# Performance work log

Measured on AMD Instinct MI355X. Metric: run time of the kernel, lower is better.

The kernel has to match this reference:

```python
import jax, jax.numpy as jnp
import numpy as np
from jax import lax

B, S, H = 2, 1024, 1024
I = 512            # moe_intermediate_size
E = 32             # n_routed_experts
TOP_K = 4
N_GROUP = 4
TOPK_GROUP = 2
SCALE = 2.5        # routed_scaling_factor
N_SHARED = 2
SH_I = I * N_SHARED


def setup_inputs() -> dict:
    key = jax.random.key(0)
    ks = jax.random.split(key, 10)
    std = 0.02
    return {
        "hidden_states": jax.random.normal(ks[0], (B, S, H), jnp.float32),
        "router_weight": jax.random.normal(ks[1], (E, H), jnp.float32) * std,
        "router_bias": jnp.zeros((E,), jnp.float32),
        "gate_w": jax.random.normal(ks[2], (E, I, H), jnp.float32) * std,
        "up_w": jax.random.normal(ks[3], (E, I, H), jnp.float32) * std,
        "down_w": jax.random.normal(ks[4], (E, H, I), jnp.float32) * std,
        "shared_gate_w": jax.random.normal(ks[5], (SH_I, H), jnp.float32) * std,
        "shared_up_w": jax.random.normal(ks[6], (SH_I, H), jnp.float32) * std,
        "shared_down_w": jax.random.normal(ks[7], (H, SH_I), jnp.float32) * std,
    }


def _route(tokens, router_weight, router_bias):
    # tokens: [T, H] -> topk_idx [T, K] int, topk_weight [T, K] f32
    logits = tokens.astype(jnp.float32) @ router_weight.astype(jnp.float32).T  # [T, E]
    scores = jax.nn.sigmoid(logits)
    sfc = scores + router_bias[None, :]
    T = tokens.shape[0]
    # group scores: sum of top-2 per group
    grp = sfc.reshape(T, N_GROUP, E // N_GROUP)
    group_scores = lax.top_k(grp, 2)[0].sum(-1)                 # [T, n_group]
    _, gidx = lax.top_k(group_scores, TOPK_GROUP)               # [T, topk_group]
    gmask = jax.nn.one_hot(gidx, N_GROUP, dtype=sfc.dtype).sum(1)  # [T, n_group]
    smask = jnp.broadcast_to(gmask[:, :, None], (T, N_GROUP, E // N_GROUP)).reshape(T, E)
    tmp = jnp.where(smask > 0, sfc, 0.0)
    _, topk_idx = lax.top_k(tmp, TOP_K)                         # [T, K]
    topk_w = jnp.take_along_axis(scores, topk_idx, axis=1)
    topk_w = topk_w / (topk_w.sum(-1, keepdims=True) + 1e-20)   # norm_topk_prob
    topk_w = topk_w * SCALE
    return topk_idx, topk_w


def reference(hidden_states, router_weight, router_bias, gate_w, up_w, down_w,
              shared_gate_w, shared_up_w, shared_down_w):
    tokens = hidden_states.reshape(-1, H)                       # [T, H]
    topk_idx, topk_w = _route(tokens, router_weight, router_bias)
    # dense all-expert SwiGLU
    gate_vals = jax.nn.silu(jnp.einsum('th,eih->tei', tokens, gate_w))
    up_vals = jnp.einsum('th,eih->tei', tokens, up_w)
    hidden_vals = gate_vals * up_vals                           # [T, E, I]
    expert_out = jnp.einsum('tei,ehi->teh', hidden_vals, down_w)  # [T, E, H]
    sel = jnp.take_along_axis(expert_out, topk_idx[:, :, None], axis=1)  # [T, K, H]
    mixed = (sel * topk_w[:, :, None].astype(sel.dtype)).sum(1)
    mixed = mixed.reshape(hidden_states.shape)
    # shared experts (dense SwiGLU MLP)
    sg = jax.nn.silu(jnp.einsum('bsh,ih->bsi', hidden_states, shared_gate_w))
    su = jnp.einsum('bsh,ih->bsi', hidden_states, shared_up_w)
    shared = jnp.einsum('bsi,hi->bsh', sg * su, shared_down_w)
    return mixed + shared
```

## Files before the change

### kernel.cpp

```cpp
#include <hip/hip_runtime.h>
#include <hip/hip_bf16.h>
#include <math.h>

#define HD 1024
#define ID 512
#define NE 32
#define NT 2048
#define NG 4
#define SHI 1024
#define SCALE 2.5f

#define BN 64
#define BK 32
#define LDA 40

typedef __bf16 bf16_t;
typedef __attribute__((ext_vector_type(8))) __bf16 bf16x8;
typedef __attribute__((ext_vector_type(4))) __bf16 bf16x4;
typedef __attribute__((ext_vector_type(4))) float f32x4;

__device__ __forceinline__ void gld16(const bf16_t* g, bf16_t* l) {
    __builtin_amdgcn_global_load_lds(
        (__attribute__((address_space(1))) void*)g,
        (__attribute__((address_space(3))) void*)l,
        16, 0, 0);
}

#define CH_G 2097152LL
#define CH_S 131072LL
#define CH_H 262144LL
#define CH_TOT (3*CH_G + 3*CH_S + CH_H)

__global__ void __launch_bounds__(256) convert_all(
    const float* __restrict__ g, const float* __restrict__ u, const float* __restrict__ d,
    const float* __restrict__ sg, const float* __restrict__ su, const float* __restrict__ sd,
    const float* __restrict__ hs, bf16_t* __restrict__ dst)
{
    for (long long c = blockIdx.x * 256LL + threadIdx.x; c < CH_TOT; c += (long long)gridDim.x * 256LL) {
        const float* src;
        long long r = c;
        if (r < CH_G)                   src = g  + (size_t)r * 8;
        else if ((r -= CH_G) < CH_G)    src = u  + (size_t)r * 8;
        else if ((r -= CH_G) < CH_G)    src = d  + (size_t)r * 8;
        else if ((r -= CH_G) < CH_S)    src = sg + (size_t)r * 8;
        else if ((r -= CH_S) < CH_S)    src = su + (size_t)r * 8;
        else if ((r -= CH_S) < CH_S)    src = sd + (size_t)r * 8;
        else { r -= CH_S;               src = hs + (size_t)r * 8; }
        float4 a = *(const float4*)src;
        float4 b = *(const float4*)(src + 4);
        bf16x8 o;
        o[0] = (__bf16)a.x; o[1] = (__bf16)a.y; o[2] = (__bf16)a.z; o[3] = (__bf16)a.w;
        o[4] = (__bf16)b.x; o[5] = (__bf16)b.y; o[6] = (__bf16)b.z; o[7] = (__bf16)b.w;
        *(bf16x8*)(dst + (size_t)c * 8) = o;
    }
}

#define LTOK 8
#define LKC 64
__global__ void __launch_bounds__(256) logits_kernel(
    const float* __restrict__ hs, const float* __restrict__ rw,
    float* __restrict__ logits, int* __restrict__ counts)
{
    if (blockIdx.x == 0 && threadIdx.x < NE) counts[threadIdx.x] = 0;

    __shared__ float Xs[LTOK][68];
    __shared__ float Ws[NE][65];

    int tid = threadIdx.x;
    int t0 = blockIdx.x * LTOK;
    int tslot = tid >> 5, ecol = tid & 31;
    float acc = 0.f;

    for (int k0 = 0; k0 < HD; k0 += LKC) {
        if (tid < 128) {
            int row = tid >> 4, q = tid & 15;
            float4 v = *(const float4*)(hs + (size_t)(t0 + row) * HD + k0 + q * 4);
            *(float4*)(&Xs[row][q * 4]) = v;
        }
        #pragma unroll
        for (int i = 0; i < 8; ++i) {
            int idx = i * 256 + tid;
            int e = idx >> 6, kk = idx & 63;
            Ws[e][kk] = rw[(size_t)e * HD + k0 + kk];
        }
        __syncthreads();
        #pragma unroll 8
        for (int kk = 0; kk < LKC; ++kk)
            acc += Xs[tslot][kk] * Ws[ecol][kk];
        __syncthreads();
    }
    logits[(size_t)(t0 + tslot) * NE + ecol] = acc;
}

__global__ void __launch_bounds__(256) topk_kernel(
    const float* __restrict__ logits, const float* __restrict__ rb,
    float* __restrict__ topkw, int* __restrict__ counts, int* __restrict__ lists)
{
    int t = blockIdx.x * 256 + threadIdx.x;
    if (t >= NT) return;

    float scores[NE], sfc[NE], tmp[NE];
    #pragma unroll
    for (int e = 0; e < NE; ++e) {
        float l = logits[(size_t)t * NE + e];
        float s = 1.f / (1.f + __expf(-l));
        scores[e] = s;
        sfc[e] = s + rb[e];
    }
    float gs[NG];
    #pragma unroll
    for (int g = 0; g < NG; ++g) {
        float m1 = -1e30f, m2 = -1e30f;
        #pragma unroll
        for (int j = 0; j < 8; ++j) {
            float v = sfc[g * 8 + j];
            if (v > m1) { m2 = m1; m1 = v; } else if (v > m2) m2 = v;
        }
        gs[g] = m1 + m2;
    }
    int g1 = 0;
    #pragma unroll
    for (int g = 1; g < NG; ++g) if (gs[g] > gs[g1]) g1 = g;
    int g2 = -1;
    #pragma unroll
    for (int g = 0; g < NG; ++g) {
        if (g == g1) continue;
        if (g2 < 0 || gs[g] > gs[g2]) g2 = g;
    }
    #pragma unroll
    for (int e = 0; e < NE; ++e) {
        int g = e >> 3;
        tmp[e] = (g == g1 || g == g2) ? sfc[e] : 0.0f;
    }
    int idx[4]; float wk[4]; float wsum = 0.f;
    #pragma unroll
    for (int k = 0; k < 4; ++k) {
        int best = 0; float bv = -1e30f;
        #pragma unroll
        for (int e = 0; e < NE; ++e) if (tmp[e] > bv) { bv = tmp[e]; best = e; }
        idx[k] = best; tmp[best] = -1e30f;
        wk[k] = scores[best]; wsum += wk[k];
    }
    float inv = SCALE / (wsum + 1e-20f);
    #pragma unroll
    for (int k = 0; k < 4; ++k) {
        int p = t * 4 + k;
        topkw[p] = wk[k] * inv;
        int e = idx[k];
        int pos = atomicAdd(&counts[e], 1);
        lists[e * NT + pos] = p;
    }
}


template<bool EXPERT, int ND, int BMT>
__global__ void __launch_bounds__(256) gateup2(
    const bf16_t* __restrict__ X, const bf16_t* __restrict__ Wg,
    const bf16_t* __restrict__ Wu, bf16_t* __restrict__ Hout,
    const int* __restrict__ lists, const int* __restrict__ counts)
{
    constexpr int NB = 64;
    int e = 0, cnt = NT;
    const bf16_t* wg = Wg; const bf16_t* wu = Wu;
    if (EXPERT) {
        e = blockIdx.x; cnt = counts[e];
        wg = Wg + (size_t)e * ND * HD;
        wu = Wu + (size_t)e * ND * HD;
    }
    int mtb = blockIdx.y, ntb = blockIdx.z;
    if (mtb * BMT >= cnt) return;

    constexpr int AU = BMT / 64;
    constexpr int MT = BMT / 32;

    __shared__ __align__(16) bf16_t As[2][BMT * BK];
    __shared__ __align__(16) bf16_t Bgs[2][NB * BK];
    __shared__ __align__(16) bf16_t Bus[2][NB * BK];
    __shared__ int rowid[BMT];

    int tid = threadIdx.x;
    if (tid < BMT) {
        int gm = mtb * BMT + tid;
        int mm = gm < cnt ? gm : cnt - 1;
        rowid[tid] = EXPERT ? lists[e * NT + mm] : mm;
    }
    __syncthreads();

    int lane = tid & 63;
    int w = tid >> 6;
    int wm = w & 1, wn = w >> 1;
    int lrow = lane & 15, quad = lane >> 4;
    int chunkL = lane & 3;

    const bf16_t* asrc[AU];
    #pragma unroll
    for (int i = 0; i < AU; ++i) {
        int row = (w * AU + i) * 16 + (lane >> 2);
        int tok = EXPERT ? (rowid[row] >> 2) : rowid[row];
        int ch = chunkL ^ ((row >> 1) & 3);
        asrc[i] = X + (size_t)tok * HD + ch * 8;
    }
    int nrow = w * 16 + (lane >> 2);
    int nch = chunkL ^ ((nrow >> 1) & 3);
    const bf16_t* bgsrc = wg + (size_t)(ntb * NB + nrow) * HD + nch * 8;
    const bf16_t* busrc = wu + (size_t)(ntb * NB + nrow) * HD + nch * 8;

    int aoff[MT], goff[2];
    #pragma unroll
    for (int mt = 0; mt < MT; ++mt) {
        int row = wm * (BMT / 2) + mt * 16 + lrow;
        aoff[mt] = row * BK + (quad ^ ((row >> 1) & 3)) * 8;
    }
    #pragma unroll
    for (int nt = 0; nt < 2; ++nt) {
        int row = wn * 32 + nt * 16 + lrow;
        goff[nt] = row * BK + (quad ^ ((row >> 1) & 3)) * 8;
    }

    f32x4 accg[MT][2], accu[MT][2];
    #pragma unroll
    for (int i = 0; i < MT; ++i)
        #pragma unroll
        for (int j = 0; j < 2; ++j) { accg[i][j] = (f32x4){0,0,0,0}; accu[i][j] = (f32x4){0,0,0,0}; }

    auto stage = [&](int buf, int k) {
        #pragma unroll
        for (int i = 0; i < AU; ++i)
            gld16(asrc[i] + k, &As[buf][(w * AU + i) * 512]);
        gld16(bgsrc + k, &Bgs[buf][w * 512]);
        gld16(busrc + k, &Bus[buf][w * 512]);
    };
    auto compute = [&](int buf) {
        bf16x8 af[MT], bg[2], bu[2];
        #pragma unroll
        for (int mt = 0; mt < MT; ++mt) af[mt] = *(const bf16x8*)(&As[buf][aoff[mt]]);
        #pragma unroll
        for (int nt = 0; nt < 2; ++nt) {
            bg[nt] = *(const bf16x8*)(&Bgs[buf][goff[nt]]);
            bu[nt] = *(const bf16x8*)(&Bus[buf][goff[nt]]);
        }
        #pragma unroll
        for (int mt = 0; mt < MT; ++mt)
            #pragma unroll
            for (int nt = 0; nt < 2; ++nt) {
                accg[mt][nt] = __builtin_amdgcn_mfma_f32_16x16x32_bf16(af[mt], bg[nt], accg[mt][nt], 0, 0, 0);
                accu[mt][nt] = __builtin_amdgcn_mfma_f32_16x16x32_bf16(af[mt], bu[nt], accu[mt][nt], 0, 0, 0);
            }
    };

    stage(0, 0);
    __syncthreads();
    int buf = 0;
    for (int k0 = BK; k0 < HD; k0 += BK) {
        stage(buf ^ 1, k0);
        compute(buf);
        __syncthreads();
        buf ^= 1;
    }
    compute(buf);

    #pragma unroll
    for (int mt = 0; mt < MT; ++mt)
        #pragma unroll
        for (int r = 0; r < 4; ++r) {
            int row_local = wm * (BMT / 2) + mt * 16 + quad * 4 + r;
            int gm = mtb * BMT + row_local;
            if (gm >= cnt) continue;
            int p = rowid[row_local];
            #pragma unroll
            for (int nt = 0; nt < 2; ++nt) {
                int col = ntb * NB + wn * 32 + nt * 16 + lrow;
                float g = accg[mt][nt][r], u = accu[mt][nt][r];
                float h = (g / (1.f + __expf(-g))) * u;
                Hout[(size_t)p * ND + col] = (__bf16)h;
            }
        }
}

template<bool EXPERT, int KD, int BMT, int NB>
__global__ void __launch_bounds__(256) down2(
    const bf16_t* __restrict__ Hin, const bf16_t* __restrict__ Wd,
    float* __restrict__ out, const int* __restrict__ lists,
    const int* __restrict__ counts, const float* __restrict__ topkw)
{
    int e = 0, cnt = NT;
    const bf16_t* wd = Wd;
    if (EXPERT) {
        e = blockIdx.x; cnt = counts[e];
        wd = Wd + (size_t)e * HD * KD;
    }
    int mtb = blockIdx.y, ntb = blockIdx.z;
    if (mtb * BMT >= cnt) return;

    constexpr int AU = BMT / 64;
    constexpr int BU = NB / 64;
    constexpr int MT = BMT / 32;
    constexpr int NTF = NB / 32;

    __shared__ __align__(16) bf16_t As[2][BMT * BK];
    __shared__ __align__(16) bf16_t Ws[2][NB * BK];
    __shared__ int rowid[BMT];

    int tid = threadIdx.x;
    if (tid < BMT) {
        int gm = mtb * BMT + tid;
        int mm = gm < cnt ? gm : cnt - 1;
        rowid[tid] = EXPERT ? lists[e * NT + mm] : mm;
    }
    __syncthreads();

    int lane = tid & 63;
    int w = tid >> 6;
    int wm = w & 1, wn = w >> 1;
    int lrow = lane & 15, quad = lane >> 4;
    int chunkL = lane & 3;

    const bf16_t* asrc[AU];
    #pragma unroll
    for (int i = 0; i < AU; ++i) {
        int row = (w * AU + i) * 16 + (lane >> 2);
        int ch = chunkL ^ ((row >> 1) & 3);
        asrc[i] = Hin + (size_t)rowid[row] * KD + ch * 8;
    }
    const bf16_t* wsrc[BU];
    #pragma unroll
    for (int i = 0; i < BU; ++i) {
        int row = (w * BU + i) * 16 + (lane >> 2);
        int ch = chunkL ^ ((row >> 1) & 3);
        wsrc[i] = wd + (size_t)(ntb * NB + row) * KD + ch * 8;
    }

    int aoff[MT], woff[NTF];
    #pragma unroll
    for (int mt = 0; mt < MT; ++mt) {
        int row = wm * (BMT / 2) + mt * 16 + lrow;
        aoff[mt] = row * BK + (quad ^ ((row >> 1) & 3)) * 8;
    }
    #pragma unroll
    for (int nt = 0; nt < NTF; ++nt) {
        int row = wn * (NB / 2) + nt * 16 + lrow;
        woff[nt] = row * BK + (quad ^ ((row >> 1) & 3)) * 8;
    }

    f32x4 acc[MT][NTF];
    #pragma unroll
    for (int i = 0; i < MT; ++i)
        #pragma unroll
        for (int j = 0; j < NTF; ++j) acc[i][j] = (f32x4){0,0,0,0};

    auto stage = [&](int buf, int k) {
        #pragma unroll
        for (int i = 0; i < AU; ++i)
            gld16(asrc[i] + k, &As[buf][(w * AU + i) * 512]);
        #pragma unroll
        for (int i = 0; i < BU; ++i)
            gld16(wsrc[i] + k, &Ws[buf][(w * BU + i) * 512]);
    };
    auto compute = [&](int buf) {
        bf16x8 af[MT], br[NTF];
        #pragma unroll
        for (int mt = 0; mt < MT; ++mt) af[mt] = *(const bf16x8*)(&As[buf][aoff[mt]]);
        #pragma unroll
        for (int nt = 0; nt < NTF; ++nt) br[nt] = *(const bf16x8*)(&Ws[buf][woff[nt]]);
        #pragma unroll
        for (int mt = 0; mt < MT; ++mt)
            #pragma unroll
            for (int nt = 0; nt < NTF; ++nt)
                acc[mt][nt] = __builtin_amdgcn_mfma_f32_16x16x32_bf16(af[mt], br[nt], acc[mt][nt], 0, 0, 0);
    };

    stage(0, 0);
    __syncthreads();
    int buf = 0;
    for (int k0 = BK; k0 < KD; k0 += BK) {
        stage(buf ^ 1, k0);
        compute(buf);
        __syncthreads();
        buf ^= 1;
    }
    compute(buf);

    #pragma unroll
    for (int mt = 0; mt < MT; ++mt)
        #pragma unroll
        for (int r = 0; r < 4; ++r) {
            int row_local = wm * (BMT / 2) + mt * 16 + quad * 4 + r;
            int gm = mtb * BMT + row_local;
            if (gm >= cnt) continue;
            int p = rowid[row_local];
            #pragma unroll
            for (int nt = 0; nt < NTF; ++nt) {
                int col = ntb * NB + wn * (NB / 2) + nt * 16 + lrow;
                float val = acc[mt][nt][r];
                if (EXPERT) {
                    float wgt = topkw[p];
                    atomicAdd(&out[(size_t)(p >> 2) * HD + col], wgt * val);
                } else {
                    out[(size_t)p * HD + col] = val;
                }
            }
        }
}


__device__ inline bf16x4 cvt4(float4 v) {
    bf16x4 r;
    r[0] = (__bf16)v.x; r[1] = (__bf16)v.y; r[2] = (__bf16)v.z; r[3] = (__bf16)v.w;
    return r;
}

template<bool EXPERT, int ND, int BMT>
__global__ void __launch_bounds__(256) gateup_mfma(
    const float* __restrict__ X, const float* __restrict__ Wg,
    const float* __restrict__ Wu, bf16_t* __restrict__ Hout,
    const int* __restrict__ lists, const int* __restrict__ counts)
{
    int e = 0, cnt = NT;
    const float* wg = Wg; const float* wu = Wu;
    if (EXPERT) {
        e = blockIdx.x; cnt = counts[e];
        wg = Wg + (size_t)e * ND * HD;
        wu = Wu + (size_t)e * ND * HD;
    }
    int mtb = blockIdx.y, ntb = blockIdx.z;
    if (mtb * BMT >= cnt) return;

    __shared__ __align__(16) bf16_t As[BMT * LDA];
    __shared__ __align__(16) bf16_t Bgs[BN * LDA];
    __shared__ __align__(16) bf16_t Bus[BN * LDA];
    __shared__ int rowid[BMT];

    int tid = threadIdx.x;
    if (tid < BMT) {
        int gm = mtb * BMT + tid;
        int mm = gm < cnt ? gm : cnt - 1;
        rowid[tid] = EXPERT ? lists[e * NT + mm] : mm;
    }
    __syncthreads();

    constexpr int AR = (BMT * BK) / (256 * 4);
    constexpr int BR = (BN * BK) / (256 * 4);
    constexpr int MT = BMT / 32;

    int lane = tid & 63;
    int w = tid >> 6;
    int wm = w & 1, wn = w >> 1;
    int lrow = lane & 15, quad = lane >> 4;

    f32x4 accg[MT][2], accu[MT][2];
    #pragma unroll
    for (int i = 0; i < MT; ++i)
        #pragma unroll
        for (int j = 0; j < 2; ++j) { accg[i][j] = (f32x4){0,0,0,0}; accu[i][j] = (f32x4){0,0,0,0}; }

    float4 pa[AR], pbg[BR], pbu[BR];

    #pragma unroll
    for (int r = 0; r < AR; ++r) {
        int idx = r * 256 + tid;
        int row = idx >> 3, kq = idx & 7;
        int tok = EXPERT ? (rowid[row] >> 2) : rowid[row];
        pa[r] = *(const float4*)(X + (size_t)tok * HD + kq * 4);
    }
    #pragma unroll
    for (int r = 0; r < BR; ++r) {
        int idx = r * 256 + tid;
        int n = idx >> 3, kq = idx & 7;
        size_t off = (size_t)(ntb * BN + n) * HD + kq * 4;
        pbg[r] = *(const float4*)(wg + off);
        pbu[r] = *(const float4*)(wu + off);
    }

    for (int k0 = 0; k0 < HD; k0 += BK) {
        #pragma unroll
        for (int r = 0; r < AR; ++r) {
            int idx = r * 256 + tid;
            int row = idx >> 3, kq = idx & 7;
            *(bf16x4*)(As + row * LDA + kq * 4) = cvt4(pa[r]);
        }
        #pragma unroll
        for (int r = 0; r < BR; ++r) {
            int idx = r * 256 + tid;
            int n = idx >> 3, kq = idx & 7;
            *(bf16x4*)(Bgs + n * LDA + kq * 4) = cvt4(pbg[r]);
            *(bf16x4*)(Bus + n * LDA + kq * 4) = cvt4(pbu[r]);
        }
        __syncthreads();

        int k1 = k0 + BK;
        if (k1 < HD) {
            #pragma unroll
            for (int r = 0; r < AR; ++r) {
                int idx = r * 256 + tid;
                int row = idx >> 3, kq = idx & 7;
                int tok = EXPERT ? (rowid[row] >> 2) : rowid[row];
                pa[r] = *(const float4*)(X + (size_t)tok * HD + k1 + kq * 4);
            }
            #pragma unroll
            for (int r = 0; r < BR; ++r) {
                int idx = r * 256 + tid;
                int n = idx >> 3, kq = idx & 7;
                size_t off = (size_t)(ntb * BN + n) * HD + k1 + kq * 4;
                pbg[r] = *(const float4*)(wg + off);
                pbu[r] = *(const float4*)(wu + off);
            }
        }

        bf16x8 af[MT], bg[2], bu[2];
        #pragma unroll
        for (int mt = 0; mt < MT; ++mt)
            af[mt] = *(const bf16x8*)(As + (wm * (BMT / 2) + mt * 16 + lrow) * LDA + quad * 8);
        #pragma unroll
        for (int nt = 0; nt < 2; ++nt) {
            bg[nt] = *(const bf16x8*)(Bgs + (wn * 32 + nt * 16 + lrow) * LDA + quad * 8);
            bu[nt] = *(const bf16x8*)(Bus + (wn * 32 + nt * 16 + lrow) * LDA + quad * 8);
        }
        #pragma unroll
        for (int mt = 0; mt < MT; ++mt)
            #pragma unroll
            for (int nt = 0; nt < 2; ++nt) {
                accg[mt][nt] = __builtin_amdgcn_mfma_f32_16x16x32_bf16(af[mt], bg[nt], accg[mt][nt], 0, 0, 0);
                accu[mt][nt] = __builtin_amdgcn_mfma_f32_16x16x32_bf16(af[mt], bu[nt], accu[mt][nt], 0, 0, 0);
            }
        __syncthreads();
    }

    #pragma unroll
    for (int mt = 0; mt < MT; ++mt)
        #pragma unroll
        for (int r = 0; r < 4; ++r) {
            int row_local = wm * (BMT / 2) + mt * 16 + quad * 4 + r;
            int gm = mtb * BMT + row_local;
            if (gm >= cnt) continue;
            int p = rowid[row_local];
            #pragma unroll
            for (int nt = 0; nt < 2; ++nt) {
                int col = ntb * BN + wn * 32 + nt * 16 + lrow;
                float g = accg[mt][nt][r], u = accu[mt][nt][r];
                float h = (g / (1.f + __expf(-g))) * u;
                Hout[(size_t)p * ND + col] = (__bf16)h;
            }
        }
}

template<bool EXPERT, int KD, int BMT>
__global__ void __launch_bounds__(256) down_mfma(
    const bf16_t* __restrict__ Hin, const float* __restrict__ Wd,
    float* __restrict__ out, const int* __restrict__ lists,
    const int* __restrict__ counts, const float* __restrict__ topkw)
{
    int e = 0, cnt = NT;
    const float* wd = Wd;
    if (EXPERT) {
        e = blockIdx.x; cnt = counts[e];
        wd = Wd + (size_t)e * HD * KD;
    }
    int mtb = blockIdx.y, ntb = blockIdx.z;
    if (mtb * BMT >= cnt) return;

    __shared__ __align__(16) bf16_t As[BMT * LDA];
    __shared__ __align__(16) bf16_t Ws[BN * LDA];
    __shared__ int rowid[BMT];

    int tid = threadIdx.x;
    if (tid < BMT) {
        int gm = mtb * BMT + tid;
        int mm = gm < cnt ? gm : cnt - 1;
        rowid[tid] = EXPERT ? lists[e * NT + mm] : mm;
    }
    __syncthreads();

    constexpr int ARH = (BMT * BK / 8) / 256;
    constexpr int BR = (BN * BK) / (256 * 4);
    constexpr int MT = BMT / 32;

    int lane = tid & 63;
    int w = tid >> 6;
    int wm = w & 1, wn = w >> 1;
    int lrow = lane & 15, quad = lane >> 4;

    f32x4 acc[MT][2];
    #pragma unroll
    for (int i = 0; i < MT; ++i)
        #pragma unroll
        for (int j = 0; j < 2; ++j) acc[i][j] = (f32x4){0,0,0,0};

    bf16x8 pa[ARH];
    float4 pw[BR];

    #pragma unroll
    for (int r = 0; r < ARH; ++r) {
        int idx = r * 256 + tid;
        int row = idx >> 2, c = idx & 3;
        pa[r] = *(const bf16x8*)(Hin + (size_t)rowid[row] * KD + c * 8);
    }
    #pragma unroll
    for (int r = 0; r < BR; ++r) {
        int idx = r * 256 + tid;
        int n = idx >> 3, kq = idx & 7;
        pw[r] = *(const float4*)(wd + (size_t)(ntb * BN + n) * KD + kq * 4);
    }

    for (int k0 = 0; k0 < KD; k0 += BK) {
        #pragma unroll
        for (int r = 0; r < ARH; ++r) {
            int idx = r * 256 + tid;
            int row = idx >> 2, c = idx & 3;
            *(bf16x8*)(As + row * LDA + c * 8) = pa[r];
        }
        #pragma unroll
        for (int r = 0; r < BR; ++r) {
            int idx = r * 256 + tid;
            int n = idx >> 3, kq = idx & 7;
            *(bf16x4*)(Ws + n * LDA + kq * 4) = cvt4(pw[r]);
        }
        __syncthreads();

        int k1 = k0 + BK;
        if (k1 < KD) {
            #pragma unroll
            for (int r = 0; r < ARH; ++r) {
                int idx = r * 256 + tid;
                int row = idx >> 2, c = idx & 3;
                pa[r] = *(const bf16x8*)(Hin + (size_t)rowid[row] * KD + k1 + c * 8);
            }
            #pragma unroll
            for (int r = 0; r < BR; ++r) {
                int idx = r * 256 + tid;
                int n = idx >> 3, kq = idx & 7;
                pw[r] = *(const float4*)(wd + (size_t)(ntb * BN + n) * KD + k1 + kq * 4);
            }
        }

        bf16x8 af[MT], bfr[2];
        #pragma unroll
        for (int mt = 0; mt < MT; ++mt)
            af[mt] = *(const bf16x8*)(As + (wm * (BMT / 2) + mt * 16 + lrow) * LDA + quad * 8);
        #pragma unroll
        for (int nt = 0; nt < 2; ++nt)
            bfr[nt] = *(const bf16x8*)(Ws + (wn * 32 + nt * 16 + lrow) * LDA + quad * 8);
        #pragma unroll
        for (int mt = 0; mt < MT; ++mt)
            #pragma unroll
            for (int nt = 0; nt < 2; ++nt)
                acc[mt][nt] = __builtin_amdgcn_mfma_f32_16x16x32_bf16(af[mt], bfr[nt], acc[mt][nt], 0, 0, 0);
        __syncthreads();
    }

    #pragma unroll
    for (int mt = 0; mt < MT; ++mt)
        #pragma unroll
        for (int r = 0; r < 4; ++r) {
            int row_local = wm * (BMT / 2) + mt * 16 + quad * 4 + r;
            int gm = mtb * BMT + row_local;
            if (gm >= cnt) continue;
            int p = rowid[row_local];
            #pragma unroll
            for (int nt = 0; nt < 2; ++nt) {
                int col = ntb * BN + wn * 32 + nt * 16 + lrow;
                float val = acc[mt][nt][r];
                if (EXPERT) {
                    float wgt = topkw[p];
                    atomicAdd(&out[(size_t)(p >> 2) * HD + col], wgt * val);
                } else {
                    out[(size_t)p * HD + col] = val;
                }
            }
        }
}

extern "C" void kernel_launch(void* const* d_in, const int* in_sizes, int n_in,
                              void* d_out, int out_size, void* d_ws, size_t ws_size,
                              hipStream_t stream) {
    const float* hs  = (const float*)d_in[0];
    const float* rw  = (const float*)d_in[1];
    const float* rb  = (const float*)d_in[2];
    const float* gw  = (const float*)d_in[3];
    const float* uw  = (const float*)d_in[4];
    const float* dw  = (const float*)d_in[5];
    const float* sgw = (const float*)d_in[6];
    const float* suw = (const float*)d_in[7];
    const float* sdw = (const float*)d_in[8];
    float* out = (float*)d_out;
    char* ws = (char*)d_ws;

    constexpr size_t BF16_ELEMS = (size_t)3 * NE * ID * HD
                                + (size_t)3 * SHI * HD
                                + (size_t)NT * HD;
    constexpr size_t REQ_WS = (size_t)(1 << 20) + BF16_ELEMS * 2 + (size_t)8192 * ID * 2;

    if (ws_size >= REQ_WS) {
        int*    counts = (int*)ws;
        float*  topkw  = (float*)(ws + 1024);
        int*    lists  = (int*)(ws + 1024 + 32768);
        float*  logits = (float*)(ws + 1024 + 32768 + 262144);

        bf16_t* wg_b = (bf16_t*)(ws + (1 << 20));
        bf16_t* wu_b = wg_b + (size_t)NE * ID * HD;
        bf16_t* wd_b = wu_b + (size_t)NE * ID * HD;
        bf16_t* sg_b = wd_b + (size_t)NE * ID * HD;
        bf16_t* su_b = sg_b + (size_t)SHI * HD;
        bf16_t* sd_b = su_b + (size_t)SHI * HD;
        bf16_t* hs_b = sd_b + (size_t)SHI * HD;
        bf16_t* hbuf = hs_b + (size_t)NT * HD;

        convert_all<<<2048, 256, 0, stream>>>(gw, uw, dw, sgw, suw, sdw, hs, wg_b);

        logits_kernel<<<NT / LTOK, 256, 0, stream>>>(hs, rw, logits, counts);
        topk_kernel<<<NT / 256, 256, 0, stream>>>(logits, rb, topkw, counts, lists);

        gateup2<false, SHI, 64><<<dim3(1, NT / 64, SHI / 64), 256, 0, stream>>>(
            hs_b, sg_b, su_b, hbuf, nullptr, nullptr);
        down2<false, SHI, 64, 64><<<dim3(1, NT / 64, HD / 64), 256, 0, stream>>>(
            hbuf, sd_b, out, nullptr, nullptr, nullptr);

        gateup2<true, ID, 128><<<dim3(NE, NT / 128, ID / 64), 256, 0, stream>>>(
            hs_b, wg_b, wu_b, hbuf, lists, counts);
        down2<true, ID, 128, 128><<<dim3(NE, NT / 128, HD / 128), 256, 0, stream>>>(
            hbuf, wd_b, out, lists, counts, topkw);
    } else {
        int*    counts = (int*)ws;
        float*  topkw  = (float*)(ws + 128);
        int*    lists  = (int*)(ws + 128 + 32768);
        float*  logits = (float*)(ws + 128 + 32768 + 262144);
        bf16_t* hbuf   = (bf16_t*)(ws + 128 + 32768 + 262144 + 262144);

        logits_kernel<<<NT / LTOK, 256, 0, stream>>>(hs, rw, logits, counts);
        topk_kernel<<<NT / 256, 256, 0, stream>>>(logits, rb, topkw, counts, lists);

        gateup_mfma<false, SHI, 64><<<dim3(1, NT / 64, SHI / BN), 256, 0, stream>>>(
            hs, sgw, suw, hbuf, nullptr, nullptr);
        down_mfma<false, SHI, 64><<<dim3(1, NT / 64, HD / BN), 256, 0, stream>>>(
            hbuf, sdw, out, nullptr, nullptr, nullptr);

        gateup_mfma<true, ID, 128><<<dim3(NE, NT / 128, ID / BN), 256, 0, stream>>>(
            hs, gw, uw, hbuf, lists, counts);
        down_mfma<true, ID, 128><<<dim3(NE, NT / 128, HD / BN), 256, 0, stream>>>(
            hbuf, dw, out, lists, counts, topkw);
    }
}
```

Before: 406.9 us.

## Merge shared and routed expert GEMMs into single launches and overlap down-weight conversion

Shared-expert and routed-expert gate/up GEMMs now run in one grid, and likewise for the down GEMMs. Both use a common 128x64 tile, and the shared path now accumulates into the output with atomics. The down-weight fp32-to-bf16 conversion moves into extra blocks of the gate/up launch so it overlaps with compute. Output zeroing is folded into the first conversion kernel, and conversion now handles 16 elements per thread. The aims are fewer launches, better GPU fill, and hiding conversion bandwidth, at the cost of extra atomic traffic for shared outputs and a separate routed hidden buffer.

```diff
diff --git a/kernel.cpp b/kernel.cpp
--- a/kernel.cpp
+++ b/kernel.cpp
@@ -13,6 +13,7 @@
 #define BN 64
 #define BK 32
 #define LDA 40
+#define NCV 4
 
 typedef __bf16 bf16_t;
 typedef __attribute__((ext_vector_type(8))) __bf16 bf16x8;
@@ -26,32 +27,46 @@
         16, 0, 0);
 }
 
-#define CH_G 2097152LL
-#define CH_S 131072LL
-#define CH_H 262144LL
-#define CH_TOT (3*CH_G + 3*CH_S + CH_H)
-
-__global__ void __launch_bounds__(256) convert_all(
-    const float* __restrict__ g, const float* __restrict__ u, const float* __restrict__ d,
-    const float* __restrict__ sg, const float* __restrict__ su, const float* __restrict__ sd,
-    const float* __restrict__ hs, bf16_t* __restrict__ dst)
+__device__ __forceinline__ void cvt16(const float* __restrict__ src, bf16_t* __restrict__ dst) {
+    float4 a0 = ((const float4*)src)[0], a1 = ((const float4*)src)[1];
+    float4 a2 = ((const float4*)src)[2], a3 = ((const float4*)src)[3];
+    bf16x8 o0, o1;
+    o0[0]=(__bf16)a0.x; o0[1]=(__bf16)a0.y; o0[2]=(__bf16)a0.z; o0[3]=(__bf16)a0.w;
+    o0[4]=(__bf16)a1.x; o0[5]=(__bf16)a1.y; o0[6]=(__bf16)a1.z; o0[7]=(__bf16)a1.w;
+    o1[0]=(__bf16)a2.x; o1[1]=(__bf16)a2.y; o1[2]=(__bf16)a2.z; o1[3]=(__bf16)a2.w;
+    o1[4]=(__bf16)a3.x; o1[5]=(__bf16)a3.y; o1[6]=(__bf16)a3.z; o1[7]=(__bf16)a3.w;
+    ((bf16x8*)dst)[0] = o0;
+    ((bf16x8*)dst)[1] = o1;
+}
+
+__global__ void __launch_bounds__(256) convert_A(
+    const float* __restrict__ g, const float* __restrict__ u,
+    const float* __restrict__ sg, const float* __restrict__ su,
+    const float* __restrict__ hs, bf16_t* __restrict__ dst,
+    float* __restrict__ outz)
 {
-    for (long long c = blockIdx.x * 256LL + threadIdx.x; c < CH_TOT; c += (long long)gridDim.x * 256LL) {
+    const long long UG = (long long)NE * ID * HD / 16;
+    const long long US = (long long)SHI * HD / 16;
+    const long long UH = (long long)NT * HD / 16;
+    const long long TOTC = 2 * UG + 2 * US + UH;
+    const long long TOT = TOTC + UH;
+    for (long long c = blockIdx.x * 256LL + threadIdx.x; c < TOT;
+         c += (long long)gridDim.x * 256LL) {
+        if (c >= TOTC) {
+            long long r = c - TOTC;
+            float4 z = {0.f, 0.f, 0.f, 0.f};
+            float4* p = (float4*)(outz + r * 16);
+            p[0] = z; p[1] = z; p[2] = z; p[3] = z;
+            continue;
+        }
         const float* src;
         long long r = c;
-        if (r < CH_G)                   src = g  + (size_t)r * 8;
-        else if ((r -= CH_G) < CH_G)    src = u  + (size_t)r * 8;
-        else if ((r -= CH_G) < CH_G)    src = d  + (size_t)r * 8;
-        else if ((r -= CH_G) < CH_S)    src = sg + (size_t)r * 8;
-        else if ((r -= CH_S) < CH_S)    src = su + (size_t)r * 8;
-        else if ((r -= CH_S) < CH_S)    src = sd + (size_t)r * 8;
-        else { r -= CH_S;               src = hs + (size_t)r * 8; }
-        float4 a = *(const float4*)src;
-        float4 b = *(const float4*)(src + 4);
-        bf16x8 o;
-        o[0] = (__bf16)a.x; o[1] = (__bf16)a.y; o[2] = (__bf16)a.z; o[3] = (__bf16)a.w;
-        o[4] = (__bf16)b.x; o[5] = (__bf16)b.y; o[6] = (__bf16)b.z; o[7] = (__bf16)b.w;
-        *(bf16x8*)(dst + (size_t)c * 8) = o;
+        if (r < UG)                   src = g  + r * 16;
+        else if ((r -= UG) < UG)      src = u  + r * 16;
+        else if ((r -= UG) < US)      src = sg + r * 16;
+        else if ((r -= US) < US)      src = su + r * 16;
+        else { r -= US;               src = hs + r * 16; }
+        cvt16(src, dst + c * 16);
     }
 }
 
@@ -153,52 +168,77 @@
 }
 
 
-template<bool EXPERT, int ND, int BMT>
-__global__ void __launch_bounds__(256) gateup2(
-    const bf16_t* __restrict__ X, const bf16_t* __restrict__ Wg,
-    const bf16_t* __restrict__ Wu, bf16_t* __restrict__ Hout,
-    const int* __restrict__ lists, const int* __restrict__ counts)
+__global__ void __launch_bounds__(256) gateup_all(
+    const bf16_t* __restrict__ hs_b,
+    const bf16_t* __restrict__ wg_b, const bf16_t* __restrict__ wu_b,
+    const bf16_t* __restrict__ sg_b, const bf16_t* __restrict__ su_b,
+    bf16_t* __restrict__ hr, bf16_t* __restrict__ hsh,
+    const int* __restrict__ lists, const int* __restrict__ counts,
+    const float* __restrict__ dwf, const float* __restrict__ sdwf,
+    bf16_t* __restrict__ dstB)
 {
-    constexpr int NB = 64;
-    int e = 0, cnt = NT;
-    const bf16_t* wg = Wg; const bf16_t* wu = Wu;
-    if (EXPERT) {
-        e = blockIdx.x; cnt = counts[e];
-        wg = Wg + (size_t)e * ND * HD;
-        wu = Wu + (size_t)e * ND * HD;
-    }
-    int mtb = blockIdx.y, ntb = blockIdx.z;
-    if (mtb * BMT >= cnt) return;
-
-    constexpr int AU = BMT / 64;
-    constexpr int MT = BMT / 32;
+    int bx = blockIdx.x, mtb = blockIdx.y, zz = blockIdx.z;
+    int tid = threadIdx.x;
+
+    if (bx >= 34) {
+        const long long UD = (long long)NE * HD * ID / 16;
+        const long long USD = (long long)HD * SHI / 16;
+        const long long TOT = UD + USD;
+        long long c = (((long long)(bx - 34) * 16 + mtb) * 8 + zz) * 256 + tid;
+        const long long stride = (long long)NCV * 128 * 256;
+        for (; c < TOT; c += stride) {
+            const float* src = (c < UD) ? (dwf + c * 16) : (sdwf + (c - UD) * 16);
+            cvt16(src, dstB + c * 16);
+        }
+        return;
+    }
+
+    constexpr int BMT = 128, NB = 64;
+    constexpr int AU = 2, MT = 4;
+
+    int cnt, ntb, ND;
+    const bf16_t *wg, *wu;
+    bf16_t* hout;
+    const int* rlist = nullptr;
+    if (bx < 32) {
+        int e = bx; cnt = counts[e];
+        if (mtb * BMT >= cnt) return;
+        ntb = zz;
+        wg = wg_b + (size_t)e * ID * HD;
+        wu = wu_b + (size_t)e * ID * HD;
+        hout = hr; ND = ID;
+        rlist = lists + e * NT;
+    } else {
+        cnt = NT;
+        ntb = (bx - 32) * 8 + zz;
+        wg = sg_b; wu = su_b;
+        hout = hsh; ND = SHI;
+    }
 
     __shared__ __align__(16) bf16_t As[2][BMT * BK];
     __shared__ __align__(16) bf16_t Bgs[2][NB * BK];
     __shared__ __align__(16) bf16_t Bus[2][NB * BK];
     __shared__ int rowid[BMT];
 
-    int tid = threadIdx.x;
     if (tid < BMT) {
         int gm = mtb * BMT + tid;
         int mm = gm < cnt ? gm : cnt - 1;
-        rowid[tid] = EXPERT ? lists[e * NT + mm] : mm;
+        rowid[tid] = rlist ? rlist[mm] : mm;
     }
     __syncthreads();
 
     int lane = tid & 63;
     int w = tid >> 6;
     int wm = w & 1, wn = w >> 1;
-    int lrow = lane & 15, quad = lane >> 4;
-    int chunkL = lane & 3;
+    int lrow = lane & 15, quad = lane >> 4, chunkL = lane & 3;
 
     const bf16_t* asrc[AU];
     #pragma unroll
     for (int i = 0; i < AU; ++i) {
         int row = (w * AU + i) * 16 + (lane >> 2);
-        int tok = EXPERT ? (rowid[row] >> 2) : rowid[row];
+        int tok = rlist ? (rowid[row] >> 2) : rowid[row];
         int ch = chunkL ^ ((row >> 1) & 3);
-        asrc[i] = X + (size_t)tok * HD + ch * 8;
+        asrc[i] = hs_b + (size_t)tok * HD + ch * 8;
     }
     int nrow = w * 16 + (lane >> 2);
     int nch = chunkL ^ ((nrow >> 1) & 3);
@@ -270,50 +310,59 @@
             #pragma unroll
             for (int nt = 0; nt < 2; ++nt) {
                 int col = ntb * NB + wn * 32 + nt * 16 + lrow;
-                float g = accg[mt][nt][r], u = accu[mt][nt][r];
-                float h = (g / (1.f + __expf(-g))) * u;
-                Hout[(size_t)p * ND + col] = (__bf16)h;
-            }
-        }
-}
-
-template<bool EXPERT, int KD, int BMT, int NB>
-__global__ void __launch_bounds__(256) down2(
-    const bf16_t* __restrict__ Hin, const bf16_t* __restrict__ Wd,
-    float* __restrict__ out, const int* __restrict__ lists,
-    const int* __restrict__ counts, const float* __restrict__ topkw)
+                float gv = accg[mt][nt][r], uv = accu[mt][nt][r];
+                float h = (gv / (1.f + __expf(-gv))) * uv;
+                hout[(size_t)p * ND + col] = (__bf16)h;
+            }
+        }
+}
+
+__global__ void __launch_bounds__(256) down_all(
+    const bf16_t* __restrict__ hr, const bf16_t* __restrict__ hsh,
+    const bf16_t* __restrict__ wd_b, const bf16_t* __restrict__ sd_b,
+    float* __restrict__ out,
+    const int* __restrict__ lists, const int* __restrict__ counts,
+    const float* __restrict__ topkw)
 {
-    int e = 0, cnt = NT;
-    const bf16_t* wd = Wd;
-    if (EXPERT) {
-        e = blockIdx.x; cnt = counts[e];
-        wd = Wd + (size_t)e * HD * KD;
-    }
-    int mtb = blockIdx.y, ntb = blockIdx.z;
-    if (mtb * BMT >= cnt) return;
-
-    constexpr int AU = BMT / 64;
-    constexpr int BU = NB / 64;
-    constexpr int MT = BMT / 32;
-    constexpr int NTF = NB / 32;
+    int bx = blockIdx.x, mtb = blockIdx.y, zz = blockIdx.z;
+    int tid = threadIdx.x;
+
+    constexpr int BMT = 128, NB = 64;
+    constexpr int AU = 2, MT = 4;
+
+    int cnt, ntb, KD;
+    const bf16_t *Hin, *wd;
+    const int* rlist = nullptr;
+    bool routed;
+    if (bx < 64) {
+        int e = bx >> 1; cnt = counts[e];
+        if (mtb * BMT >= cnt) return;
+        ntb = (bx & 1) * 8 + zz;
+        Hin = hr; wd = wd_b + (size_t)e * HD * ID; KD = ID;
+        rlist = lists + e * NT;
+        routed = true;
+    } else {
+        cnt = NT;
+        ntb = (bx - 64) * 8 + zz;
+        Hin = hsh; wd = sd_b; KD = SHI;
+        routed = false;
+    }
 
     __shared__ __align__(16) bf16_t As[2][BMT * BK];
     __shared__ __align__(16) bf16_t Ws[2][NB * BK];
     __shared__ int rowid[BMT];
 
-    int tid = threadIdx.x;
     if (tid < BMT) {
         int gm = mtb * BMT + tid;
         int mm = gm < cnt ? gm : cnt - 1;
-        rowid[tid] = EXPERT ? lists[e * NT + mm] : mm;
+        rowid[tid] = rlist ? rlist[mm] : mm;
     }
     __syncthreads();
 
     int lane = tid & 63;
     int w = tid >> 6;
     int wm = w & 1, wn = w >> 1;
-    int lrow = lane & 15, quad = lane >> 4;
-    int chunkL = lane & 3;
+    int lrow = lane & 15, quad = lane >> 4, chunkL = lane & 3;
 
     const bf16_t* asrc[AU];
     #pragma unroll
@@ -322,50 +371,44 @@
         int ch = chunkL ^ ((row >> 1) & 3);
         asrc[i] = Hin + (size_t)rowid[row] * KD + ch * 8;
     }
-    const bf16_t* wsrc[BU];
-    #pragma unroll
-    for (int i = 0; i < BU; ++i) {
-        int row = (w * BU + i) * 16 + (lane >> 2);
-        int ch = chunkL ^ ((row >> 1) & 3);
-        wsrc[i] = wd + (size_t)(ntb * NB + row) * KD + ch * 8;
-    }
-
-    int aoff[MT], woff[NTF];
+    int nrow = w * 16 + (lane >> 2);
+    int nch = chunkL ^ ((nrow >> 1) & 3);
+    const bf16_t* wsrc = wd + (size_t)(ntb * NB + nrow) * KD + nch * 8;
+
+    int aoff[MT], woff[2];
     #pragma unroll
     for (int mt = 0; mt < MT; ++mt) {
         int row = wm * (BMT / 2) + mt * 16 + lrow;
         aoff[mt] = row * BK + (quad ^ ((row >> 1) & 3)) * 8;
     }
     #pragma unroll
-    for (int nt = 0; nt < NTF; ++nt) {
-        int row = wn * (NB / 2) + nt * 16 + lrow;
+    for (int nt = 0; nt < 2; ++nt) {
+        int row = wn * 32 + nt * 16 + lrow;
         woff[nt] = row * BK + (quad ^ ((row >> 1) & 3)) * 8;
     }
 
-    f32x4 acc[MT][NTF];
+    f32x4 acc[MT][2];
     #pragma unroll
     for (int i = 0; i < MT; ++i)
         #pragma unroll
-        for (int j = 0; j < NTF; ++j) acc[i][j] = (f32x4){0,0,0,0};
+        for (int j = 0; j < 2; ++j) acc[i][j] = (f32x4){0,0,0,0};
 
     auto stage = [&](int buf, int k) {
         #pragma unroll
         for (int i = 0; i < AU; ++i)
             gld16(asrc[i] + k, &As[buf][(w * AU + i) * 512]);
-        #pragma unroll
-        for (int i = 0; i < BU; ++i)
-            gld16(wsrc[i] + k, &Ws[buf][(w * BU + i) * 512]);
+        gld16(wsrc + k, &Ws[buf][w * 512]);
     };
     auto compute = [&](int buf) {
-        bf16x8 af[MT], br[NTF];
+        bf16x8 af[MT], br[2];
         #pragma unroll
         for (int mt = 0; mt < MT; ++mt) af[mt] = *(const bf16x8*)(&As[buf][aoff[mt]]);
         #pragma unroll
-        for (int nt = 0; nt < NTF; ++nt) br[nt] = *(const bf16x8*)(&Ws[buf][woff[nt]]);
+        for (int nt = 0; nt < 2; ++nt) br[nt] = *(const bf16x8*)(&Ws[buf][woff[nt]]);
         #pragma unroll
         for (int mt = 0; mt < MT; ++mt)
             #pragma unroll
-            for (int nt = 0; nt < NTF; ++nt)
+            for (int nt = 0; nt < 2; ++nt)
                 acc[mt][nt] = __builtin_amdgcn_mfma_f32_16x16x32_bf16(af[mt], br[nt], acc[mt][nt], 0, 0, 0);
     };
 
@@ -389,14 +432,14 @@
             if (gm >= cnt) continue;
             int p = rowid[row_local];
             #pragma unroll
-            for (int nt = 0; nt < NTF; ++nt) {
-                int col = ntb * NB + wn * (NB / 2) + nt * 16 + lrow;
+            for (int nt = 0; nt < 2; ++nt) {
+                int col = ntb * NB + wn * 32 + nt * 16 + lrow;
                 float val = acc[mt][nt][r];
-                if (EXPERT) {
+                if (routed) {
                     float wgt = topkw[p];
                     atomicAdd(&out[(size_t)(p >> 2) * HD + col], wgt * val);
                 } else {
-                    out[(size_t)p * HD + col] = val;
+                    atomicAdd(&out[(size_t)p * HD + col], val);
                 }
             }
         }
@@ -684,10 +727,11 @@
     float* out = (float*)d_out;
     char* ws = (char*)d_ws;
 
-    constexpr size_t BF16_ELEMS = (size_t)3 * NE * ID * HD
-                                + (size_t)3 * SHI * HD
-                                + (size_t)NT * HD;
-    constexpr size_t REQ_WS = (size_t)(1 << 20) + BF16_ELEMS * 2 + (size_t)8192 * ID * 2;
+    constexpr size_t MIR_A = 2 * (size_t)NE * ID * HD + 2 * (size_t)SHI * HD + (size_t)NT * HD;
+    constexpr size_t MIR_B = (size_t)NE * ID * HD + (size_t)SHI * HD;
+    constexpr size_t HR_E  = (size_t)NT * 4 * ID;
+    constexpr size_t HSH_E = (size_t)NT * SHI;
+    constexpr size_t REQ_WS = (size_t)(1 << 20) + (MIR_A + MIR_B + HR_E + HSH_E) * 2;
 
     if (ws_size >= REQ_WS) {
         int*    counts = (int*)ws;
@@ -695,29 +739,24 @@
         int*    lists  = (int*)(ws + 1024 + 32768);
         float*  logits = (float*)(ws + 1024 + 32768 + 262144);
 
-        bf16_t* wg_b = (bf16_t*)(ws + (1 << 20));
+        bf16_t* mir  = (bf16_t*)(ws + (1 << 20));
+        bf16_t* wg_b = mir;
         bf16_t* wu_b = wg_b + (size_t)NE * ID * HD;
-        bf16_t* wd_b = wu_b + (size_t)NE * ID * HD;
-        bf16_t* sg_b = wd_b + (size_t)NE * ID * HD;
+        bf16_t* sg_b = wu_b + (size_t)NE * ID * HD;
         bf16_t* su_b = sg_b + (size_t)SHI * HD;
-        bf16_t* sd_b = su_b + (size_t)SHI * HD;
-        bf16_t* hs_b = sd_b + (size_t)SHI * HD;
-        bf16_t* hbuf = hs_b + (size_t)NT * HD;
-
-        convert_all<<<2048, 256, 0, stream>>>(gw, uw, dw, sgw, suw, sdw, hs, wg_b);
+        bf16_t* hs_b = su_b + (size_t)SHI * HD;
+        bf16_t* wd_b = hs_b + (size_t)NT * HD;
+        bf16_t* sd_b = wd_b + (size_t)NE * ID * HD;
+        bf16_t* hr   = sd_b + (size_t)SHI * HD;
+        bf16_t* hsh  = hr + HR_E;
 
         logits_kernel<<<NT / LTOK, 256, 0, stream>>>(hs, rw, logits, counts);
         topk_kernel<<<NT / 256, 256, 0, stream>>>(logits, rb, topkw, counts, lists);
-
-        gateup2<false, SHI, 64><<<dim3(1, NT / 64, SHI / 64), 256, 0, stream>>>(
-            hs_b, sg_b, su_b, hbuf, nullptr, nullptr);
-        down2<false, SHI, 64, 64><<<dim3(1, NT / 64, HD / 64), 256, 0, stream>>>(
-            hbuf, sd_b, out, nullptr, nullptr, nullptr);
-
-        gateup2<true, ID, 128><<<dim3(NE, NT / 128, ID / 64), 256, 0, stream>>>(
-            hs_b, wg_b, wu_b, hbuf, lists, counts);
-        down2<true, ID, 128, 128><<<dim3(NE, NT / 128, HD / 128), 256, 0, stream>>>(
-            hbuf, wd_b, out, lists, counts, topkw);
+        convert_A<<<2048, 256, 0, stream>>>(gw, uw, sgw, suw, hs, mir, out);
+        gateup_all<<<dim3(34 + NCV, 16, 8), 256, 0, stream>>>(
+            hs_b, wg_b, wu_b, sg_b, su_b, hr, hsh, lists, counts, dw, sdw, wd_b);
+        down_all<<<dim3(66, 16, 8), 256, 0, stream>>>(
+            hr, hsh, wd_b, sd_b, out, lists, counts, topkw);
     } else {
         int*    counts = (int*)ws;
         float*  topkw  = (float*)(ws + 128);
```

Measured after the change: 395.6 us. -2.8%, faster.
